# Performance work log

Measured on AMD Instinct MI355X. Metric: run time of the kernel, lower is better.

## Reference

```python
import jax, jax.numpy as jnp
import numpy as np

D_IN, D_HID, D_CLS, N_CLASSES = 1024, 256, 128, 4
CELL_IN = 512
N = 50000


def setup_inputs() -> dict:
    key = jax.random.key(0)
    ks = jax.random.split(key, 20)
    s = 0.02
    inp = {
        "x_path": jax.random.normal(ks[0], (1, N, D_IN), jnp.float32),
        "x_cell": jax.random.normal(ks[1], (1, N, CELL_IN), jnp.float32),
        # wsi_net / cell_net projections
        "wsi_w": jax.random.normal(ks[2], (D_IN, D_HID), jnp.float32) * s,
        "wsi_b": jnp.zeros((D_HID,), jnp.float32),
        "cell_w": jax.random.normal(ks[3], (CELL_IN, D_HID), jnp.float32) * s,
        "cell_b": jnp.zeros((D_HID,), jnp.float32),
        # cross-attention Q/K/V
        "wq_w": jax.random.normal(ks[4], (D_HID, D_HID), jnp.float32) * s,
        "wq_b": jnp.zeros((D_HID,), jnp.float32),
        "wk_w": jax.random.normal(ks[5], (D_HID, D_HID), jnp.float32) * s,
        "wk_b": jnp.zeros((D_HID,), jnp.float32),
        "wv_w": jax.random.normal(ks[6], (D_HID, D_HID), jnp.float32) * s,
        "wv_b": jnp.zeros((D_HID,), jnp.float32),
        # gated attention (L=D=256, n_classes=1)
        "aa_w": jax.random.normal(ks[7], (D_HID, D_HID), jnp.float32) * s,
        "aa_b": jnp.zeros((D_HID,), jnp.float32),
        "ab_w": jax.random.normal(ks[8], (D_HID, D_HID), jnp.float32) * s,
        "ab_b": jnp.zeros((D_HID,), jnp.float32),
        "ac_w": jax.random.normal(ks[9], (D_HID, 1), jnp.float32) * s,
        "ac_b": jnp.zeros((1,), jnp.float32),
        # classifier MLP
        "c1_w": jax.random.normal(ks[10], (D_HID, D_CLS), jnp.float32) * s,
        "c1_b": jnp.zeros((D_CLS,), jnp.float32),
        "c2_w": jax.random.normal(ks[11], (D_CLS, N_CLASSES), jnp.float32) * s,
        "c2_b": jnp.zeros((N_CLASSES,), jnp.float32),
    }
    return inp


def reference(x_path, x_cell, wsi_w, wsi_b, cell_w, cell_b,
              wq_w, wq_b, wk_w, wk_b, wv_w, wv_b,
              aa_w, aa_b, ab_w, ab_b, ac_w, ac_b,
              c1_w, c1_b, c2_w, c2_b):
    xp = x_path[0]            # (N, D_IN)
    xc = x_cell[0]            # (N, CELL_IN)
    # instance-level projections (dropout inactive at eval)
    h_path = jax.nn.relu(xp @ wsi_w + wsi_b)    # (N, d)
    h_cell = jax.nn.relu(xc @ cell_w + cell_b)  # (N, d)
    # cross attention with per-instance seq_len=1 (bmm over N singleton batches)
    q = h_cell @ wq_w + wq_b
    k = h_path @ wk_w + wk_b
    v = h_path @ wv_w + wv_b
    scores = (jnp.einsum('nd,nd->n', q, k) / jnp.sqrt(jnp.float32(q.shape[-1])))[:, None, None]  # (N,1,1)
    attn_w = jax.nn.softmax(scores, axis=-1)     # (N,1,1), trivially ones
    fused = attn_w[:, 0, :] * v                  # (N, d)
    # gated attention MIL pooling
    a = jnp.tanh(fused @ aa_w + aa_b)
    b = jax.nn.sigmoid(fused @ ab_w + ab_b)
    A = (a * b) @ ac_w + ac_b                    # (N, 1)
    A_t = A.T                                    # (1, N)
    pooled = jax.nn.softmax(A_t, axis=1) @ fused # (1, d)
    # classifier MLP
    risk = jax.nn.relu(pooled @ c1_w + c1_b) @ c2_w + c2_b  # (1, n_classes)
    return risk
```

## Files before the change

kernel.cpp:

```cpp
#include <hip/hip_runtime.h>
#include <hip/hip_bf16.h>
#include <math.h>

#define D_IN 1024
#define D_HID 256
#define D_CLS 128
#define N_CLASSES 4
#define N_INST 50000

#define NPAD 50176
#define G1I (NPAD / 32)
#define RG2 128
#define GB (NPAD / RG2)
#define PSTR 258
#define NEG_BIG (-1e30f)

#define ROWS 64
#define NBLK ((N_INST + ROWS - 1) / ROWS)
#define NB2 64
#define CHUNK ((NBLK + NB2 - 1) / NB2)

#define WS_W1T   0u
#define WS_WVT   524288u
#define WS_WAT   655360u
#define WS_WBT   786432u
#define WS_CNT   917504u
#define WS_P1    917760u
#define WS_H     1322304u
#define WS_NEED2 ((size_t)WS_H + 25690112u)
#define WS_P1F   917504u
#define WS_P2F   1724800u

typedef __attribute__((ext_vector_type(8))) short bf16x8;
typedef __attribute__((ext_vector_type(4))) float f32x4;

__device__ __forceinline__ short f2bf(float x) {
    __hip_bfloat16 h = __float2bfloat16(x);
    return *reinterpret_cast<short*>(&h);
}
__device__ __forceinline__ float fast_tanh(float x) {
    float e = __expf(2.f * x);
    return 1.f - 2.f * __builtin_amdgcn_rcpf(e + 1.f);
}
__device__ __forceinline__ float fast_sigmoid(float x) {
    return __builtin_amdgcn_rcpf(1.f + __expf(-x));
}
__device__ __forceinline__ bf16x8 cvt8(float4 a, float4 b) {
    bf16x8 r;
    r[0] = f2bf(a.x); r[1] = f2bf(a.y); r[2] = f2bf(a.z); r[3] = f2bf(a.w);
    r[4] = f2bf(b.x); r[5] = f2bf(b.y); r[6] = f2bf(b.z); r[7] = f2bf(b.w);
    return r;
}
__device__ __forceinline__ bf16x8 cvt8v(f32x4 a, f32x4 b) {
    bf16x8 r;
    r[0] = f2bf(a[0]); r[1] = f2bf(a[1]); r[2] = f2bf(a[2]); r[3] = f2bf(a[3]);
    r[4] = f2bf(b[0]); r[5] = f2bf(b[1]); r[6] = f2bf(b[2]); r[7] = f2bf(b[3]);
    return r;
}
__device__ __forceinline__ bf16x8 load_cvt8(const float* __restrict__ p) {
    return cvt8(*(const float4*)p, *(const float4*)(p + 4));
}
__device__ __forceinline__ void async_ld16(const float* g, float* l) {
    __builtin_amdgcn_global_load_lds(
        (const __attribute__((address_space(1))) void*)g,
        (__attribute__((address_space(3))) void*)l, 16, 0, 0);
}

__global__ void convert_weights(const float* __restrict__ w1, const float* __restrict__ wv,
                                const float* __restrict__ wa, const float* __restrict__ wb,
                                __hip_bfloat16* __restrict__ w1t, __hip_bfloat16* __restrict__ wvt,
                                __hip_bfloat16* __restrict__ wat, __hip_bfloat16* __restrict__ wbt,
                                int frag) {
    __shared__ __hip_bfloat16 T[64][68];
    int b = blockIdx.x, tid = threadIdx.x;
    if (frag && b < 64) {
        const int group = tid >> 6, lane = tid & 63;
        const int colb = lane & 15;
        const int kb = (lane >> 4) * 8;
#pragma unroll
        for (int p = 0; p < 2; p++) {
            int tile = b * 8 + group * 2 + p;
            int kc = tile >> 4, w = (tile >> 2) & 3, ct = tile & 3;
            int col = w * 64 + ct * 16 + colb;
            const float* s = w1 + (size_t)(kc * 32 + kb) * D_HID + col;
            bf16x8 o;
#pragma unroll
            for (int j = 0; j < 8; j++) o[j] = f2bf(s[(size_t)j * D_HID]);
            *(bf16x8*)(w1t + (size_t)tile * 512 + lane * 8) = o;
        }
        return;
    }
    const float* src; __hip_bfloat16* dst; int K, tr, tc;
    if (b < 64) { src = w1; dst = w1t; K = D_IN; tr = b >> 2; tc = b & 3; }
    else {
        int m = (b - 64) >> 4, t = (b - 64) & 15;
        src = (m == 0) ? wv : (m == 1) ? wa : wb;
        dst = (m == 0) ? wvt : (m == 1) ? wat : wbt;
        K = D_HID; tr = t >> 2; tc = t & 3;
    }
    int k0 = tr * 64, n0 = tc * 64;
#pragma unroll
    for (int p = 0; p < 4; p++) {
        int lin = p * 256 + tid;
        int r = lin >> 4;
        int c4 = (lin & 15) << 2;
        float4 v = *(const float4*)(src + (size_t)(k0 + r) * D_HID + n0 + c4);
        T[c4 + 0][r] = __float2bfloat16(v.x);
        T[c4 + 1][r] = __float2bfloat16(v.y);
        T[c4 + 2][r] = __float2bfloat16(v.z);
        T[c4 + 3][r] = __float2bfloat16(v.w);
    }
    __syncthreads();
#pragma unroll
    for (int p = 0; p < 4; p++) {
        int lin = p * 256 + tid;
        int n = lin >> 4;
        int kq = (lin & 15) << 2;
        ushort4 o;
        o.x = *(unsigned short*)&T[n][kq + 0];
        o.y = *(unsigned short*)&T[n][kq + 1];
        o.z = *(unsigned short*)&T[n][kq + 2];
        o.w = *(unsigned short*)&T[n][kq + 3];
        *(ushort4*)(dst + (size_t)(n0 + n) * K + k0 + kq) = o;
    }
}

__global__ __launch_bounds__(256, 5) void mcat_stage1i(const float* __restrict__ xp,
                                                       const __hip_bfloat16* __restrict__ w1f,
                                                       const float* __restrict__ b1,
                                                       __hip_bfloat16* __restrict__ hout) {
    __shared__ float Xs[4][1024];

    const int tid  = threadIdx.x;
    const int wave = tid >> 6;
    const int lane = tid & 63;
    const int quad = lane >> 4;
    const int l16  = lane & 15;
    const int row0 = blockIdx.x * 32;
    const int t128 = blockIdx.x >> 2;
    const int qtr  = blockIdx.x & 3;

    const int rsub = lane >> 3;
    const int gran = (lane & 7) ^ rsub;
    const float* xsrc;
    {
        int rg = row0 + wave * 8 + rsub;
        if (rg > N_INST - 1) rg = N_INST - 1;
        xsrc = xp + (size_t)rg * D_IN + gran * 4;
    }

    const __hip_bfloat16* wbase = w1f + (size_t)wave * 4 * 512 + lane * 8;

    f32x4 acc[2][4];
    f32x4 zero = {0.f, 0.f, 0.f, 0.f};
#pragma unroll
    for (int i = 0; i < 2; i++)
#pragma unroll
        for (int j = 0; j < 4; j++) acc[i][j] = zero;

    async_ld16(xsrc + 0, &Xs[0][wave * 256]);
    bf16x8 wcur[4];
#pragma unroll
    for (int ct = 0; ct < 4; ct++) wcur[ct] = *(const bf16x8*)(wbase + (size_t)ct * 512);
    async_ld16(xsrc + 32, &Xs[1][wave * 256]);
    async_ld16(xsrc + 64, &Xs[2][wave * 256]);

    const int key = l16 & 7;
#pragma unroll 1
    for (int t = 0; t < 32; t++) {
        if (t == 0)      asm volatile("s_waitcnt vmcnt(2)" ::: "memory");
        else if (t < 29) asm volatile("s_waitcnt vmcnt(1)" ::: "memory");
        else             asm volatile("s_waitcnt vmcnt(0)" ::: "memory");
        __builtin_amdgcn_s_barrier();

        bf16x8 wnx[4];
        if (t < 31) {
#pragma unroll
            for (int ct = 0; ct < 4; ct++)
                wnx[ct] = *(const bf16x8*)(wbase + (size_t)((t + 1) * 16 + ct) * 512);
        }
        if (t < 29) async_ld16(xsrc + (t + 3) * 32, &Xs[(t + 3) & 3][wave * 256]);

        const float* bufp = &Xs[t & 3][0];
#pragma unroll
        for (int rt = 0; rt < 2; rt++) {
            const float* rp = bufp + (rt * 16 + l16) * 32;
            f32x4 lo = *(const f32x4*)(rp + (((2 * quad) ^ key) << 2));
            f32x4 hi = *(const f32x4*)(rp + (((2 * quad + 1) ^ key) << 2));
            bf16x8 af = cvt8v(lo, hi);
#pragma unroll
            for (int ct = 0; ct < 4; ct++)
                acc[rt][ct] = __builtin_amdgcn_mfma_f32_16x16x32_bf16(af, wcur[ct], acc[rt][ct], 0, 0, 0);
        }
        if (t < 31) {
#pragma unroll
            for (int ct = 0; ct < 4; ct++) wcur[ct] = wnx[ct];
        }
    }

#pragma unroll
    for (int ct = 0; ct < 4; ct++) {
        const int col = wave * 64 + ct * 16 + l16;
        const float bias = b1[col];
        __hip_bfloat16* hb = hout + (((size_t)(t128 * 8 + (col >> 5)) * 4 + ((col >> 3) & 3)) << 10)
                                  + qtr * 256 + (col & 7);
#pragma unroll
        for (int rt = 0; rt < 2; rt++)
#pragma unroll
            for (int r = 0; r < 4; r++) {
                int row = rt * 16 + quad * 4 + r;
                hb[row * 8] = __float2bfloat16(fmaxf(acc[rt][ct][r] + bias, 0.f));
            }
    }
}

__global__ __launch_bounds__(512, 1) void mcat_stage2(const __hip_bfloat16* __restrict__ h,
                          const __hip_bfloat16* __restrict__ wvt, const float* __restrict__ bv,
                          const __hip_bfloat16* __restrict__ wat, const float* __restrict__ ba,
                          const __hip_bfloat16* __restrict__ wbt, const float* __restrict__ bb,
                          const float* __restrict__ acw, const float* __restrict__ acb,
                          float* __restrict__ p1, unsigned int* __restrict__ counter,
                          const float* __restrict__ c1w, const float* __restrict__ c1b,
                          const float* __restrict__ c2w, const float* __restrict__ c2b,
                          float* __restrict__ out) {
    __shared__ __hip_bfloat16 Vs[RG2][264];
    __shared__ float Apart[8][RG2];
    __shared__ float ExpW[RG2];
    __shared__ float smx[4];
    __shared__ float scb[GB];
    __shared__ float pooled[D_HID];
    __shared__ float r1v[D_CLS];

    const int tid  = threadIdx.x;
    const int wave = tid >> 6;
    const int lane = tid & 63;
    const int quad = lane >> 4;
    const int l16  = lane & 15;
    const int cb   = wave * 32;
    const int row0 = blockIdx.x * RG2;

    f32x4 acc[8][2];
    f32x4 zero = {0.f, 0.f, 0.f, 0.f};

    const __hip_bfloat16* hb = h + (size_t)blockIdx.x * 32768 + quad * 1024 + l16 * 8;
#pragma unroll
    for (int i = 0; i < 8; i++) { acc[i][0] = zero; acc[i][1] = zero; }
    {
        const __hip_bfloat16* w0 = wvt + (size_t)(cb + l16) * D_HID + quad * 8;
        const __hip_bfloat16* w1p = w0 + 16 * D_HID;
#pragma unroll
        for (int ks = 0; ks < 8; ks++) {
            bf16x8 b0 = *(const bf16x8*)(w0 + ks * 32);
            bf16x8 b1f = *(const bf16x8*)(w1p + ks * 32);
#pragma unroll
            for (int rt = 0; rt < 8; rt++) {
                bf16x8 af = *(const bf16x8*)(hb + ks * 4096 + rt * 128);
                acc[rt][0] = __builtin_amdgcn_mfma_f32_16x16x32_bf16(af, b0, acc[rt][0], 0, 0, 0);
                acc[rt][1] = __builtin_amdgcn_mfma_f32_16x16x32_bf16(af, b1f, acc[rt][1], 0, 0, 0);
            }
        }
    }
#pragma unroll
    for (int ct = 0; ct < 2; ct++) {
        int col = cb + ct * 16 + l16;
        float bias = bv[col];
#pragma unroll
        for (int rt = 0; rt < 8; rt++)
#pragma unroll
            for (int r = 0; r < 4; r++)
                Vs[rt * 16 + quad * 4 + r][col] = __float2bfloat16(acc[rt][ct][r] + bias);
    }
    __syncthreads();

    float a_reg[8][2][4];
#pragma unroll
    for (int i = 0; i < 8; i++) { acc[i][0] = zero; acc[i][1] = zero; }
    {
        const __hip_bfloat16* w0 = wat + (size_t)(cb + l16) * D_HID + quad * 8;
        const __hip_bfloat16* w1p = w0 + 16 * D_HID;
#pragma unroll
        for (int ks = 0; ks < 8; ks++) {
            bf16x8 b0 = *(const bf16x8*)(w0 + ks * 32);
            bf16x8 b1f = *(const bf16x8*)(w1p + ks * 32);
#pragma unroll
            for (int rt = 0; rt < 8; rt++) {
                bf16x8 af = *(const bf16x8*)&Vs[rt * 16 + l16][ks * 32 + quad * 8];
                acc[rt][0] = __builtin_amdgcn_mfma_f32_16x16x32_bf16(af, b0, acc[rt][0], 0, 0, 0);
                acc[rt][1] = __builtin_amdgcn_mfma_f32_16x16x32_bf16(af, b1f, acc[rt][1], 0, 0, 0);
            }
        }
    }
#pragma unroll
    for (int ct = 0; ct < 2; ct++) {
        float bias = ba[cb + ct * 16 + l16];
#pragma unroll
        for (int rt = 0; rt < 8; rt++)
#pragma unroll
            for (int r = 0; r < 4; r++)
                a_reg[rt][ct][r] = fast_tanh(acc[rt][ct][r] + bias);
    }

#pragma unroll
    for (int i = 0; i < 8; i++) { acc[i][0] = zero; acc[i][1] = zero; }
    {
        const __hip_bfloat16* w0 = wbt + (size_t)(cb + l16) * D_HID + quad * 8;
        const __hip_bfloat16* w1p = w0 + 16 * D_HID;
#pragma unroll
        for (int ks = 0; ks < 8; ks++) {
            bf16x8 b0 = *(const bf16x8*)(w0 + ks * 32);
            bf16x8 b1f = *(const bf16x8*)(w1p + ks * 32);
#pragma unroll
            for (int rt = 0; rt < 8; rt++) {
                bf16x8 af = *(const bf16x8*)&Vs[rt * 16 + l16][ks * 32 + quad * 8];
                acc[rt][0] = __builtin_amdgcn_mfma_f32_16x16x32_bf16(af, b0, acc[rt][0], 0, 0, 0);
                acc[rt][1] = __builtin_amdgcn_mfma_f32_16x16x32_bf16(af, b1f, acc[rt][1], 0, 0, 0);
            }
        }
    }
    {
        float acw0 = acw[cb + l16], acw1 = acw[cb + 16 + l16];
        float bb0 = bb[cb + l16],  bb1 = bb[cb + 16 + l16];
        float sp[8][4];
#pragma unroll
        for (int rt = 0; rt < 8; rt++)
#pragma unroll
            for (int r = 0; r < 4; r++) {
                float g0 = a_reg[rt][0][r] * fast_sigmoid(acc[rt][0][r] + bb0);
                float g1 = a_reg[rt][1][r] * fast_sigmoid(acc[rt][1][r] + bb1);
                sp[rt][r] = g0 * acw0 + g1 * acw1;
            }
#pragma unroll
        for (int off = 1; off < 16; off <<= 1)
#pragma unroll
            for (int rt = 0; rt < 8; rt++)
#pragma unroll
                for (int r = 0; r < 4; r++)
                    sp[rt][r] += __shfl_xor(sp[rt][r], off, 16);
        if (l16 == 0) {
#pragma unroll
            for (int rt = 0; rt < 8; rt++)
#pragma unroll
                for (int r = 0; r < 4; r++)
                    Apart[wave][rt * 16 + quad * 4 + r] = sp[rt][r];
        }
    }
    __syncthreads();

    if (tid < 64) {
        float A0 = acb[0], A1 = acb[0];
#pragma unroll
        for (int w = 0; w < 8; w++) { A0 += Apart[w][tid]; A1 += Apart[w][tid + 64]; }
        bool v0 = (row0 + tid) < N_INST;
        bool v1 = (row0 + 64 + tid) < N_INST;
        if (!v0) A0 = NEG_BIG;
        if (!v1) A1 = NEG_BIG;
        float m = fmaxf(A0, A1);
#pragma unroll
        for (int off = 32; off > 0; off >>= 1) m = fmaxf(m, __shfl_xor(m, off));
        float e0 = v0 ? __expf(A0 - m) : 0.f;
        float e1 = v1 ? __expf(A1 - m) : 0.f;
        ExpW[tid] = e0; ExpW[tid + 64] = e1;
        float ssum = e0 + e1;
#pragma unroll
        for (int off = 32; off > 0; off >>= 1) ssum += __shfl_xor(ssum, off);
        if (tid == 0) {
            p1[(size_t)blockIdx.x * PSTR + 0] = m;
            p1[(size_t)blockIdx.x * PSTR + 1] = ssum;
        }
    }
    __syncthreads();
    if (tid < 256) {
        float p = 0.f;
#pragma unroll 8
        for (int n = 0; n < RG2; n++)
            p += ExpW[n] * __bfloat162float(Vs[n][tid]);
        p1[(size_t)blockIdx.x * PSTR + 2 + tid] = p;
    }

    __syncthreads();
    if (tid == 0) {
        __threadfence();
        unsigned int old = __hip_atomic_fetch_add(counter, 1u, __ATOMIC_ACQ_REL, __HIP_MEMORY_SCOPE_AGENT);
        smx[3] = (old == GB - 1) ? 1.f : 0.f;
    }
    __syncthreads();
    if (smx[3] == 0.f) return;
    __threadfence();

    {
        float mloc = NEG_BIG;
        for (int b = tid; b < GB; b += 512) mloc = fmaxf(mloc, p1[(size_t)b * PSTR]);
#pragma unroll
        for (int off = 32; off > 0; off >>= 1) mloc = fmaxf(mloc, __shfl_xor(mloc, off));
        if (lane == 0) ExpW[wave] = mloc;
    }
    __syncthreads();
    if (tid == 0) {
        float M = NEG_BIG;
#pragma unroll
        for (int w = 0; w < 8; w++) M = fmaxf(M, ExpW[w]);
        smx[0] = M;
    }
    __syncthreads();
    {
        float M = smx[0];
        float sl = 0.f;
        for (int b = tid; b < GB; b += 512) {
            float s = __expf(p1[(size_t)b * PSTR] - M);
            scb[b] = s;
            sl += s * p1[(size_t)b * PSTR + 1];
        }
#pragma unroll
        for (int off = 32; off > 0; off >>= 1) sl += __shfl_xor(sl, off);
        if (lane == 0) ExpW[8 + wave] = sl;
    }
    __syncthreads();
    if (tid == 0) {
        float S = 0.f;
#pragma unroll
        for (int w = 0; w < 8; w++) S += ExpW[8 + w];
        smx[1] = S;
    }
    __syncthreads();
    if (tid < 256) {
        float p = 0.f;
        for (int b = 0; b < GB; b++)
            p += scb[b] * p1[(size_t)b * PSTR + 2 + tid];
        pooled[tid] = p / smx[1];
    }
    __syncthreads();
    if (tid < D_CLS) {
        float a2 = c1b[tid];
#pragma unroll 8
        for (int d = 0; d < D_HID; d++)
            a2 += pooled[d] * c1w[(size_t)d * D_CLS + tid];
        r1v[tid] = fmaxf(a2, 0.f);
    }
    __syncthreads();
    if (tid < N_CLASSES) {
        float a2 = c2b[tid];
#pragma unroll 8
        for (int j = 0; j < D_CLS; j++)
            a2 += r1v[j] * c2w[(size_t)j * N_CLASSES + tid];
        out[tid] = a2;
    }
}

__device__ __forceinline__ void gemm256_w8(const __hip_bfloat16 (*S)[264],
                                           const __hip_bfloat16* __restrict__ Wt,
                                           int colbase, int quad, int l16, f32x4 acc[4][2]) {
    f32x4 zero = {0.f, 0.f, 0.f, 0.f};
#pragma unroll
    for (int i = 0; i < 4; i++) { acc[i][0] = zero; acc[i][1] = zero; }
    const __hip_bfloat16* w0 = Wt + (size_t)(colbase + l16) * D_HID + quad * 8;
    const __hip_bfloat16* w1 = w0 + 16 * D_HID;
#pragma unroll
    for (int ks = 0; ks < 8; ks++) {
        bf16x8 af[4];
#pragma unroll
        for (int rt = 0; rt < 4; rt++)
            af[rt] = *(const bf16x8*)&S[rt * 16 + l16][ks * 32 + quad * 8];
        bf16x8 b0 = *(const bf16x8*)(w0 + ks * 32);
        bf16x8 b1 = *(const bf16x8*)(w1 + ks * 32);
#pragma unroll
        for (int rt = 0; rt < 4; rt++) {
            acc[rt][0] = __builtin_amdgcn_mfma_f32_16x16x32_bf16(af[rt], b0, acc[rt][0], 0, 0, 0);
            acc[rt][1] = __builtin_amdgcn_mfma_f32_16x16x32_bf16(af[rt], b1, acc[rt][1], 0, 0, 0);
        }
    }
}

__global__ __launch_bounds__(512, 4) void mcat_mainF(const float* __restrict__ xsrc,
                          const __hip_bfloat16* __restrict__ w1t, const float* __restrict__ b1,
                          const __hip_bfloat16* __restrict__ wvt, const float* __restrict__ bv,
                          const __hip_bfloat16* __restrict__ wat, const float* __restrict__ ba,
                          const __hip_bfloat16* __restrict__ wbt, const float* __restrict__ bb,
                          const float* __restrict__ acw, const float* __restrict__ acb,
                          float* __restrict__ partials) {
    __shared__ __hip_bfloat16 Hs[ROWS][264];
    __shared__ __hip_bfloat16 Vs[ROWS][264];
    __shared__ float Apart[8][ROWS];
    __shared__ float ExpW[ROWS];
    const int tid  = threadIdx.x;
    const int wave = tid >> 6;
    const int lane = tid & 63;
    const int quad = lane >> 4;
    const int l16  = lane & 15;
    const int colbase = wave * 32;
    const int row0 = blockIdx.x * ROWS;
    f32x4 acc[4][2];
    f32x4 zero = {0.f, 0.f, 0.f, 0.f};
#pragma unroll
    for (int i = 0; i < 4; i++) { acc[i][0] = zero; acc[i][1] = zero; }
    const float* xf_base[4];
#pragma unroll
    for (int rt = 0; rt < 4; rt++) {
        int r = row0 + rt * 16 + l16;
        if (r > N_INST - 1) r = N_INST - 1;
        xf_base[rt] = xsrc + (size_t)r * D_IN + quad * 8;
    }
    const __hip_bfloat16* wb0 = w1t + (size_t)(colbase + l16) * D_IN + quad * 8;
    const __hip_bfloat16* wb1 = wb0 + 16 * D_IN;
    for (int kc = 0; kc < D_IN; kc += 32) {
        bf16x8 af[4];
#pragma unroll
        for (int rt = 0; rt < 4; rt++) af[rt] = load_cvt8(xf_base[rt] + kc);
        bf16x8 b0 = *(const bf16x8*)(wb0 + kc);
        bf16x8 b1 = *(const bf16x8*)(wb1 + kc);
#pragma unroll
        for (int rt = 0; rt < 4; rt++) {
            acc[rt][0] = __builtin_amdgcn_mfma_f32_16x16x32_bf16(af[rt], b0, acc[rt][0], 0, 0, 0);
            acc[rt][1] = __builtin_amdgcn_mfma_f32_16x16x32_bf16(af[rt], b1, acc[rt][1], 0, 0, 0);
        }
    }
#pragma unroll
    for (int ct = 0; ct < 2; ct++) {
        int col = colbase + ct * 16 + l16;
        float bias = b1[col];
#pragma unroll
        for (int rt = 0; rt < 4; rt++)
#pragma unroll
            for (int r = 0; r < 4; r++)
                Hs[rt * 16 + quad * 4 + r][col] = __float2bfloat16(fmaxf(acc[rt][ct][r] + bias, 0.f));
    }
    __syncthreads();
    gemm256_w8(Hs, wvt, colbase, quad, l16, acc);
#pragma unroll
    for (int ct = 0; ct < 2; ct++) {
        int col = colbase + ct * 16 + l16;
        float bias = bv[col];
#pragma unroll
        for (int rt = 0; rt < 4; rt++)
#pragma unroll
            for (int r = 0; r < 4; r++)
                Vs[rt * 16 + quad * 4 + r][col] = __float2bfloat16(acc[rt][ct][r] + bias);
    }
    __syncthreads();
    float a_reg[4][2][4];
    gemm256_w8(Vs, wat, colbase, quad, l16, acc);
#pragma unroll
    for (int ct = 0; ct < 2; ct++) {
        float bias = ba[colbase + ct * 16 + l16];
#pragma unroll
        for (int rt = 0; rt < 4; rt++)
#pragma unroll
            for (int r = 0; r < 4; r++)
                a_reg[rt][ct][r] = fast_tanh(acc[rt][ct][r] + bias);
    }
    gemm256_w8(Vs, wbt, colbase, quad, l16, acc);
    {
        float acw0 = acw[colbase + l16];
        float acw1 = acw[colbase + 16 + l16];
        float bias0 = bb[colbase + l16];
        float bias1 = bb[colbase + 16 + l16];
        float sp[4][4];
#pragma unroll
        for (int rt = 0; rt < 4; rt++)
#pragma unroll
            for (int r = 0; r < 4; r++) {
                float g0 = a_reg[rt][0][r] * fast_sigmoid(acc[rt][0][r] + bias0);
                float g1 = a_reg[rt][1][r] * fast_sigmoid(acc[rt][1][r] + bias1);
                sp[rt][r] = g0 * acw0 + g1 * acw1;
            }
#pragma unroll
        for (int off = 1; off < 16; off <<= 1)
#pragma unroll
            for (int rt = 0; rt < 4; rt++)
#pragma unroll
                for (int r = 0; r < 4; r++)
                    sp[rt][r] += __shfl_xor(sp[rt][r], off, 16);
        if (l16 == 0) {
#pragma unroll
            for (int rt = 0; rt < 4; rt++)
#pragma unroll
                for (int r = 0; r < 4; r++)
                    Apart[wave][rt * 16 + quad * 4 + r] = sp[rt][r];
        }
    }
    __syncthreads();
    if (tid < 64) {
        bool valid = (row0 + tid) < N_INST;
        float A = acb[0];
#pragma unroll
        for (int w = 0; w < 8; w++) A += Apart[w][tid];
        if (!valid) A = NEG_BIG;
        float m = A;
#pragma unroll
        for (int off = 32; off > 0; off >>= 1) m = fmaxf(m, __shfl_xor(m, off));
        float e = valid ? __expf(A - m) : 0.f;
        ExpW[tid] = e;
        float ssum = e;
#pragma unroll
        for (int off = 32; off > 0; off >>= 1) ssum += __shfl_xor(ssum, off);
        if (tid == 0) {
            partials[(size_t)blockIdx.x * PSTR + 0] = m;
            partials[(size_t)blockIdx.x * PSTR + 1] = ssum;
        }
    }
    __syncthreads();
    if (tid < 256) {
        float p = 0.f;
#pragma unroll 8
        for (int n = 0; n < 64; n++)
            p += ExpW[n] * __bfloat162float(Vs[n][tid]);
        partials[(size_t)blockIdx.x * PSTR + 2 + tid] = p;
    }
}

__global__ void mcat_fin_a(const float* __restrict__ p1, float* __restrict__ p2) {
    __shared__ float sm[1];
    int g = blockIdx.x, tid = threadIdx.x;
    int lo = g * CHUNK;
    int hi = lo + CHUNK; if (hi > NBLK) hi = NBLK;
    if (tid < 64) {
        float m = NEG_BIG;
        if (lo + tid < hi) m = p1[(size_t)(lo + tid) * PSTR];
#pragma unroll
        for (int off = 32; off > 0; off >>= 1) m = fmaxf(m, __shfl_xor(m, off));
        if (tid == 0) sm[0] = m;
    }
    __syncthreads();
    float M = sm[0];
    float p = 0.f, sacc = 0.f;
    for (int b = lo; b < hi; b++) {
        float sc = __expf(p1[(size_t)b * PSTR] - M);
        sacc += sc * p1[(size_t)b * PSTR + 1];
        p += sc * p1[(size_t)b * PSTR + 2 + tid];
    }
    if (tid == 0) {
        p2[(size_t)g * PSTR + 0] = M;
        p2[(size_t)g * PSTR + 1] = sacc;
    }
    p2[(size_t)g * PSTR + 2 + tid] = p;
}

__global__ void mcat_fin_b(const float* __restrict__ p2,
                           const float* __restrict__ c1w, const float* __restrict__ c1b,
                           const float* __restrict__ c2w, const float* __restrict__ c2b,
                           float* __restrict__ out) {
    __shared__ float sm[2];
    __shared__ float sc[NB2];
    __shared__ float pooled[D_HID];
    __shared__ float r1[D_CLS];
    int tid = threadIdx.x;
    if (tid < 64) {
        float m = p2[(size_t)tid * PSTR];
#pragma unroll
        for (int off = 32; off > 0; off >>= 1) m = fmaxf(m, __shfl_xor(m, off));
        if (tid == 0) sm[0] = m;
    }
    __syncthreads();
    float M = sm[0];
    if (tid < 64) {
        float s = __expf(p2[(size_t)tid * PSTR] - M);
        sc[tid] = s;
        float Ssum = s * p2[(size_t)tid * PSTR + 1];
#pragma unroll
        for (int off = 32; off > 0; off >>= 1) Ssum += __shfl_xor(Ssum, off);
        if (tid == 0) sm[1] = Ssum;
    }
    __syncthreads();
    float S = sm[1];
    float p = 0.f;
#pragma unroll 8
    for (int b = 0; b < NB2; b++)
        p += sc[b] * p2[(size_t)b * PSTR + 2 + tid];
    pooled[tid] = p / S;
    __syncthreads();
    if (tid < D_CLS) {
        float acc = c1b[tid];
#pragma unroll 8
        for (int d = 0; d < D_HID; d++)
            acc += pooled[d] * c1w[(size_t)d * D_CLS + tid];
        r1[tid] = fmaxf(acc, 0.f);
    }
    __syncthreads();
    if (tid < N_CLASSES) {
        float acc = c2b[tid];
#pragma unroll 8
        for (int j = 0; j < D_CLS; j++)
            acc += r1[j] * c2w[(size_t)j * N_CLASSES + tid];
        out[tid] = acc;
    }
}

extern "C" void kernel_launch(void* const* d_in, const int* in_sizes, int n_in,
                              void* d_out, int out_size, void* d_ws, size_t ws_size,
                              hipStream_t stream) {
    const float* xp  = (const float*)d_in[0];
    const float* w1  = (const float*)d_in[2];
    const float* b1  = (const float*)d_in[3];
    const float* wv  = (const float*)d_in[10];
    const float* bv  = (const float*)d_in[11];
    const float* wa  = (const float*)d_in[12];
    const float* ba  = (const float*)d_in[13];
    const float* wb  = (const float*)d_in[14];
    const float* bb  = (const float*)d_in[15];
    const float* acw = (const float*)d_in[16];
    const float* acb = (const float*)d_in[17];
    const float* c1w = (const float*)d_in[18];
    const float* c1b = (const float*)d_in[19];
    const float* c2w = (const float*)d_in[20];
    const float* c2b = (const float*)d_in[21];
    float* out = (float*)d_out;

    char* ws = (char*)d_ws;
    __hip_bfloat16* w1t = (__hip_bfloat16*)(ws + WS_W1T);
    __hip_bfloat16* wvt = (__hip_bfloat16*)(ws + WS_WVT);
    __hip_bfloat16* wat = (__hip_bfloat16*)(ws + WS_WAT);
    __hip_bfloat16* wbt = (__hip_bfloat16*)(ws + WS_WBT);

    const int use_main = (ws_size >= WS_NEED2) ? 1 : 0;
    hipLaunchKernelGGL(convert_weights, dim3(112), dim3(256), 0, stream,
                       w1, wv, wa, wb, w1t, wvt, wat, wbt, use_main);

    if (use_main) {
        unsigned int* counter = (unsigned int*)(ws + WS_CNT);
        float* p1 = (float*)(ws + WS_P1);
        __hip_bfloat16* h  = (__hip_bfloat16*)(ws + WS_H);
        hipMemsetAsync(counter, 0, 4, stream);
        hipLaunchKernelGGL(mcat_stage1i, dim3(G1I), dim3(256), 0, stream, xp, w1t, b1, h);
        hipLaunchKernelGGL(mcat_stage2, dim3(GB), dim3(512), 0, stream,
                           h, wvt, bv, wat, ba, wbt, bb, acw, acb, p1, counter,
                           c1w, c1b, c2w, c2b, out);
    } else {
        float* p1 = (float*)(ws + WS_P1F);
        float* p2 = (float*)(ws + WS_P2F);
        hipLaunchKernelGGL(mcat_mainF, dim3(NBLK), dim3(512), 0, stream,
                           xp, w1t, b1, wvt, bv, wat, ba, wbt, bb, acw, acb, p1);
        hipLaunchKernelGGL(mcat_fin_a, dim3(NB2), dim3(256), 0, stream, p1, p2);
        hipLaunchKernelGGL(mcat_fin_b, dim3(1), dim3(256), 0, stream,
                           p2, c1w, c1b, c2w, c2b, out);
    }
}
```

Baseline: 509.7 us.

## Fuse stage1 projection with V/gate stages into one 32-row kernel

Merges the two-kernel main path into a single kernel. Each 32-row block now computes relu(x@W1), keeps H in shared memory, then runs the V, tanh and sigmoid gate projections and the per-block softmax partials. This removes the bf16 H round trip through global memory and one launch. In exchange it uses more LDS and registers (occupancy hint lowered to 3), repeats the small-weight loads in 4x more blocks, and makes the last-block final reduction handle 4x more partials.

After: 583.3 us. 14.4% more time.

```diff
diff --git a/kernel.cpp b/kernel.cpp
--- a/kernel.cpp
+++ b/kernel.cpp
@@ -10,8 +10,6 @@
 
 #define NPAD 50176
 #define G1I (NPAD / 32)
-#define RG2 128
-#define GB (NPAD / RG2)
 #define PSTR 258
 #define NEG_BIG (-1e30f)
 
@@ -26,8 +24,7 @@
 #define WS_WBT   786432u
 #define WS_CNT   917504u
 #define WS_P1    917760u
-#define WS_H     1322304u
-#define WS_NEED2 ((size_t)WS_H + 25690112u)
+#define WS_NEEDF ((size_t)WS_P1 + 1618176u)
 #define WS_P1F   917504u
 #define WS_P2F   1724800u
 
@@ -73,20 +70,28 @@
                                 int frag) {
     __shared__ __hip_bfloat16 T[64][68];
     int b = blockIdx.x, tid = threadIdx.x;
-    if (frag && b < 64) {
+    if (frag) {
         const int group = tid >> 6, lane = tid & 63;
         const int colb = lane & 15;
         const int kb = (lane >> 4) * 8;
+        const float* src; __hip_bfloat16* dst; int tbase;
+        if (b < 64) { src = w1; dst = w1t; tbase = b * 8; }
+        else {
+            int m = (b - 64) >> 4;
+            src = (m == 0) ? wv : (m == 1) ? wa : wb;
+            dst = (m == 0) ? wvt : (m == 1) ? wat : wbt;
+            tbase = ((b - 64) & 15) * 8;
+        }
 #pragma unroll
         for (int p = 0; p < 2; p++) {
-            int tile = b * 8 + group * 2 + p;
+            int tile = tbase + group * 2 + p;
             int kc = tile >> 4, w = (tile >> 2) & 3, ct = tile & 3;
             int col = w * 64 + ct * 16 + colb;
-            const float* s = w1 + (size_t)(kc * 32 + kb) * D_HID + col;
+            const float* s = src + (size_t)(kc * 32 + kb) * D_HID + col;
             bf16x8 o;
 #pragma unroll
             for (int j = 0; j < 8; j++) o[j] = f2bf(s[(size_t)j * D_HID]);
-            *(bf16x8*)(w1t + (size_t)tile * 512 + lane * 8) = o;
+            *(bf16x8*)(dst + (size_t)tile * 512 + lane * 8) = o;
         }
         return;
     }
@@ -125,11 +130,26 @@
     }
 }
 
-__global__ __launch_bounds__(256, 5) void mcat_stage1i(const float* __restrict__ xp,
-                                                       const __hip_bfloat16* __restrict__ w1f,
-                                                       const float* __restrict__ b1,
-                                                       __hip_bfloat16* __restrict__ hout) {
-    __shared__ float Xs[4][1024];
+__global__ __launch_bounds__(256, 3) void mcat_fused(const float* __restrict__ xp,
+                          const __hip_bfloat16* __restrict__ w1f, const float* __restrict__ b1,
+                          const __hip_bfloat16* __restrict__ wvf, const float* __restrict__ bv,
+                          const __hip_bfloat16* __restrict__ waf, const float* __restrict__ ba,
+                          const __hip_bfloat16* __restrict__ wbf, const float* __restrict__ bbp,
+                          const float* __restrict__ acw, const float* __restrict__ acb,
+                          float* __restrict__ p1, unsigned int* __restrict__ counter,
+                          const float* __restrict__ c1w, const float* __restrict__ c1b,
+                          const float* __restrict__ c2w, const float* __restrict__ c2b,
+                          float* __restrict__ out) {
+    __shared__ __align__(16) char smem[50832];
+    float (*Xs)[1024]          = (float (*)[1024])smem;
+    __hip_bfloat16 (*Hs)[264]  = (__hip_bfloat16 (*)[264])(smem + 16384);
+    __hip_bfloat16 (*Vsh)[264] = (__hip_bfloat16 (*)[264])(smem + 33280);
+    float (*Apart)[32]         = (float (*)[32])(smem + 50176);
+    float* ExpW = (float*)(smem + 50688);
+    float* smx  = (float*)(smem + 50816);
+    float* scb    = (float*)smem;
+    float* pooled = (float*)(smem + 8192);
+    float* r1v    = (float*)(smem + 9216);
 
     const int tid  = threadIdx.x;
     const int wave = tid >> 6;
@@ -137,8 +157,7 @@
     const int quad = lane >> 4;
     const int l16  = lane & 15;
     const int row0 = blockIdx.x * 32;
-    const int t128 = blockIdx.x >> 2;
-    const int qtr  = blockIdx.x & 3;
+    const int colb = wave * 64;
 
     const int rsub = lane >> 3;
     const int gran = (lane & 7) ^ rsub;
@@ -148,7 +167,6 @@
         if (rg > N_INST - 1) rg = N_INST - 1;
         xsrc = xp + (size_t)rg * D_IN + gran * 4;
     }
-
     const __hip_bfloat16* wbase = w1f + (size_t)wave * 4 * 512 + lane * 8;
 
     f32x4 acc[2][4];
@@ -200,145 +218,131 @@
 
 #pragma unroll
     for (int ct = 0; ct < 4; ct++) {
-        const int col = wave * 64 + ct * 16 + l16;
+        const int col = colb + ct * 16 + l16;
         const float bias = b1[col];
-        __hip_bfloat16* hb = hout + (((size_t)(t128 * 8 + (col >> 5)) * 4 + ((col >> 3) & 3)) << 10)
-                                  + qtr * 256 + (col & 7);
 #pragma unroll
         for (int rt = 0; rt < 2; rt++)
 #pragma unroll
+            for (int r = 0; r < 4; r++)
+                Hs[rt * 16 + quad * 4 + r][col] = __float2bfloat16(fmaxf(acc[rt][ct][r] + bias, 0.f));
+    }
+    __syncthreads();
+
+    f32x4 vacc[2][4];
+#pragma unroll
+    for (int i = 0; i < 2; i++)
+#pragma unroll
+        for (int j = 0; j < 4; j++) vacc[i][j] = zero;
+    {
+        const __hip_bfloat16* wvb = wvf + (size_t)wave * 4 * 512 + lane * 8;
+#pragma unroll
+        for (int kc = 0; kc < 8; kc++) {
+            bf16x8 wfr[4];
+#pragma unroll
+            for (int ct = 0; ct < 4; ct++)
+                wfr[ct] = *(const bf16x8*)(wvb + (size_t)(kc * 16 + ct) * 512);
+#pragma unroll
+            for (int rt = 0; rt < 2; rt++) {
+                bf16x8 af = *(const bf16x8*)&Hs[rt * 16 + l16][kc * 32 + quad * 8];
+#pragma unroll
+                for (int ct = 0; ct < 4; ct++)
+                    vacc[rt][ct] = __builtin_amdgcn_mfma_f32_16x16x32_bf16(af, wfr[ct], vacc[rt][ct], 0, 0, 0);
+            }
+        }
+    }
+#pragma unroll
+    for (int ct = 0; ct < 4; ct++) {
+        const int col = colb + ct * 16 + l16;
+        const float bias = bv[col];
+#pragma unroll
+        for (int rt = 0; rt < 2; rt++)
+#pragma unroll
+            for (int r = 0; r < 4; r++)
+                Vsh[rt * 16 + quad * 4 + r][col] = __float2bfloat16(vacc[rt][ct][r] + bias);
+    }
+    __syncthreads();
+
+#pragma unroll
+    for (int i = 0; i < 2; i++)
+#pragma unroll
+        for (int j = 0; j < 4; j++) vacc[i][j] = zero;
+    {
+        const __hip_bfloat16* wab = waf + (size_t)wave * 4 * 512 + lane * 8;
+#pragma unroll
+        for (int kc = 0; kc < 8; kc++) {
+            bf16x8 wfr[4];
+#pragma unroll
+            for (int ct = 0; ct < 4; ct++)
+                wfr[ct] = *(const bf16x8*)(wab + (size_t)(kc * 16 + ct) * 512);
+#pragma unroll
+            for (int rt = 0; rt < 2; rt++) {
+                bf16x8 af = *(const bf16x8*)&Vsh[rt * 16 + l16][kc * 32 + quad * 8];
+#pragma unroll
+                for (int ct = 0; ct < 4; ct++)
+                    vacc[rt][ct] = __builtin_amdgcn_mfma_f32_16x16x32_bf16(af, wfr[ct], vacc[rt][ct], 0, 0, 0);
+            }
+        }
+    }
+    float a_reg[2][4][4];
+#pragma unroll
+    for (int ct = 0; ct < 4; ct++) {
+        const float bias = ba[colb + ct * 16 + l16];
+#pragma unroll
+        for (int rt = 0; rt < 2; rt++)
+#pragma unroll
+            for (int r = 0; r < 4; r++)
+                a_reg[rt][ct][r] = fast_tanh(vacc[rt][ct][r] + bias);
+    }
+
+#pragma unroll
+    for (int i = 0; i < 2; i++)
+#pragma unroll
+        for (int j = 0; j < 4; j++) vacc[i][j] = zero;
+    {
+        const __hip_bfloat16* wbb = wbf + (size_t)wave * 4 * 512 + lane * 8;
+#pragma unroll
+        for (int kc = 0; kc < 8; kc++) {
+            bf16x8 wfr[4];
+#pragma unroll
+            for (int ct = 0; ct < 4; ct++)
+                wfr[ct] = *(const bf16x8*)(wbb + (size_t)(kc * 16 + ct) * 512);
+#pragma unroll
+            for (int rt = 0; rt < 2; rt++) {
+                bf16x8 af = *(const bf16x8*)&Vsh[rt * 16 + l16][kc * 32 + quad * 8];
+#pragma unroll
+                for (int ct = 0; ct < 4; ct++)
+                    vacc[rt][ct] = __builtin_amdgcn_mfma_f32_16x16x32_bf16(af, wfr[ct], vacc[rt][ct], 0, 0, 0);
+            }
+        }
+    }
+    {
+        float acwv[4], bbv[4];
+#pragma unroll
+        for (int ct = 0; ct < 4; ct++) {
+            acwv[ct] = acw[colb + ct * 16 + l16];
+            bbv[ct]  = bbp[colb + ct * 16 + l16];
+        }
+        float sp[2][4];
+#pragma unroll
+        for (int rt = 0; rt < 2; rt++)
+#pragma unroll
             for (int r = 0; r < 4; r++) {
-                int row = rt * 16 + quad * 4 + r;
-                hb[row * 8] = __float2bfloat16(fmaxf(acc[rt][ct][r] + bias, 0.f));
+                float s = 0.f;
+#pragma unroll
+                for (int ct = 0; ct < 4; ct++)
+                    s += a_reg[rt][ct][r] * fast_sigmoid(vacc[rt][ct][r] + bbv[ct]) * acwv[ct];
+                sp[rt][r] = s;
             }
-    }
-}
-
-__global__ __launch_bounds__(512, 1) void mcat_stage2(const __hip_bfloat16* __restrict__ h,
-                          const __hip_bfloat16* __restrict__ wvt, const float* __restrict__ bv,
-                          const __hip_bfloat16* __restrict__ wat, const float* __restrict__ ba,
-                          const __hip_bfloat16* __restrict__ wbt, const float* __restrict__ bb,
-                          const float* __restrict__ acw, const float* __restrict__ acb,
-                          float* __restrict__ p1, unsigned int* __restrict__ counter,
-                          const float* __restrict__ c1w, const float* __restrict__ c1b,
-                          const float* __restrict__ c2w, const float* __restrict__ c2b,
-                          float* __restrict__ out) {
-    __shared__ __hip_bfloat16 Vs[RG2][264];
-    __shared__ float Apart[8][RG2];
-    __shared__ float ExpW[RG2];
-    __shared__ float smx[4];
-    __shared__ float scb[GB];
-    __shared__ float pooled[D_HID];
-    __shared__ float r1v[D_CLS];
-
-    const int tid  = threadIdx.x;
-    const int wave = tid >> 6;
-    const int lane = tid & 63;
-    const int quad = lane >> 4;
-    const int l16  = lane & 15;
-    const int cb   = wave * 32;
-    const int row0 = blockIdx.x * RG2;
-
-    f32x4 acc[8][2];
-    f32x4 zero = {0.f, 0.f, 0.f, 0.f};
-
-    const __hip_bfloat16* hb = h + (size_t)blockIdx.x * 32768 + quad * 1024 + l16 * 8;
-#pragma unroll
-    for (int i = 0; i < 8; i++) { acc[i][0] = zero; acc[i][1] = zero; }
-    {
-        const __hip_bfloat16* w0 = wvt + (size_t)(cb + l16) * D_HID + quad * 8;
-        const __hip_bfloat16* w1p = w0 + 16 * D_HID;
-#pragma unroll
-        for (int ks = 0; ks < 8; ks++) {
-            bf16x8 b0 = *(const bf16x8*)(w0 + ks * 32);
-            bf16x8 b1f = *(const bf16x8*)(w1p + ks * 32);
-#pragma unroll
-            for (int rt = 0; rt < 8; rt++) {
-                bf16x8 af = *(const bf16x8*)(hb + ks * 4096 + rt * 128);
-                acc[rt][0] = __builtin_amdgcn_mfma_f32_16x16x32_bf16(af, b0, acc[rt][0], 0, 0, 0);
-                acc[rt][1] = __builtin_amdgcn_mfma_f32_16x16x32_bf16(af, b1f, acc[rt][1], 0, 0, 0);
-            }
-        }
-    }
-#pragma unroll
-    for (int ct = 0; ct < 2; ct++) {
-        int col = cb + ct * 16 + l16;
-        float bias = bv[col];
-#pragma unroll
-        for (int rt = 0; rt < 8; rt++)
-#pragma unroll
-            for (int r = 0; r < 4; r++)
-                Vs[rt * 16 + quad * 4 + r][col] = __float2bfloat16(acc[rt][ct][r] + bias);
-    }
-    __syncthreads();
-
-    float a_reg[8][2][4];
-#pragma unroll
-    for (int i = 0; i < 8; i++) { acc[i][0] = zero; acc[i][1] = zero; }
-    {
-        const __hip_bfloat16* w0 = wat + (size_t)(cb + l16) * D_HID + quad * 8;
-        const __hip_bfloat16* w1p = w0 + 16 * D_HID;
-#pragma unroll
-        for (int ks = 0; ks < 8; ks++) {
-            bf16x8 b0 = *(const bf16x8*)(w0 + ks * 32);
-            bf16x8 b1f = *(const bf16x8*)(w1p + ks * 32);
-#pragma unroll
-            for (int rt = 0; rt < 8; rt++) {
-                bf16x8 af = *(const bf16x8*)&Vs[rt * 16 + l16][ks * 32 + quad * 8];
-                acc[rt][0] = __builtin_amdgcn_mfma_f32_16x16x32_bf16(af, b0, acc[rt][0], 0, 0, 0);
-                acc[rt][1] = __builtin_amdgcn_mfma_f32_16x16x32_bf16(af, b1f, acc[rt][1], 0, 0, 0);
-            }
-        }
-    }
-#pragma unroll
-    for (int ct = 0; ct < 2; ct++) {
-        float bias = ba[cb + ct * 16 + l16];
-#pragma unroll
-        for (int rt = 0; rt < 8; rt++)
-#pragma unroll
-            for (int r = 0; r < 4; r++)
-                a_reg[rt][ct][r] = fast_tanh(acc[rt][ct][r] + bias);
-    }
-
-#pragma unroll
-    for (int i = 0; i < 8; i++) { acc[i][0] = zero; acc[i][1] = zero; }
-    {
-        const __hip_bfloat16* w0 = wbt + (size_t)(cb + l16) * D_HID + quad * 8;
-        const __hip_bfloat16* w1p = w0 + 16 * D_HID;
-#pragma unroll
-        for (int ks = 0; ks < 8; ks++) {
-            bf16x8 b0 = *(const bf16x8*)(w0 + ks * 32);
-            bf16x8 b1f = *(const bf16x8*)(w1p + ks * 32);
-#pragma unroll
-            for (int rt = 0; rt < 8; rt++) {
-                bf16x8 af = *(const bf16x8*)&Vs[rt * 16 + l16][ks * 32 + quad * 8];
-                acc[rt][0] = __builtin_amdgcn_mfma_f32_16x16x32_bf16(af, b0, acc[rt][0], 0, 0, 0);
-                acc[rt][1] = __builtin_amdgcn_mfma_f32_16x16x32_bf16(af, b1f, acc[rt][1], 0, 0, 0);
-            }
-        }
-    }
-    {
-        float acw0 = acw[cb + l16], acw1 = acw[cb + 16 + l16];
-        float bb0 = bb[cb + l16],  bb1 = bb[cb + 16 + l16];
-        float sp[8][4];
-#pragma unroll
-        for (int rt = 0; rt < 8; rt++)
-#pragma unroll
-            for (int r = 0; r < 4; r++) {
-                float g0 = a_reg[rt][0][r] * fast_sigmoid(acc[rt][0][r] + bb0);
-                float g1 = a_reg[rt][1][r] * fast_sigmoid(acc[rt][1][r] + bb1);
-                sp[rt][r] = g0 * acw0 + g1 * acw1;
-            }
 #pragma unroll
         for (int off = 1; off < 16; off <<= 1)
 #pragma unroll
-            for (int rt = 0; rt < 8; rt++)
+            for (int rt = 0; rt < 2; rt++)
 #pragma unroll
                 for (int r = 0; r < 4; r++)
                     sp[rt][r] += __shfl_xor(sp[rt][r], off, 16);
         if (l16 == 0) {
 #pragma unroll
-            for (int rt = 0; rt < 8; rt++)
+            for (int rt = 0; rt < 2; rt++)
 #pragma unroll
                 for (int r = 0; r < 4; r++)
                     Apart[wave][rt * 16 + quad * 4 + r] = sp[rt][r];
@@ -346,34 +350,31 @@
     }
     __syncthreads();
 
-    if (tid < 64) {
-        float A0 = acb[0], A1 = acb[0];
-#pragma unroll
-        for (int w = 0; w < 8; w++) { A0 += Apart[w][tid]; A1 += Apart[w][tid + 64]; }
-        bool v0 = (row0 + tid) < N_INST;
-        bool v1 = (row0 + 64 + tid) < N_INST;
-        if (!v0) A0 = NEG_BIG;
-        if (!v1) A1 = NEG_BIG;
-        float m = fmaxf(A0, A1);
-#pragma unroll
-        for (int off = 32; off > 0; off >>= 1) m = fmaxf(m, __shfl_xor(m, off));
-        float e0 = v0 ? __expf(A0 - m) : 0.f;
-        float e1 = v1 ? __expf(A1 - m) : 0.f;
-        ExpW[tid] = e0; ExpW[tid + 64] = e1;
-        float ssum = e0 + e1;
-#pragma unroll
-        for (int off = 32; off > 0; off >>= 1) ssum += __shfl_xor(ssum, off);
+    if (tid < 32) {
+        float A = acb[0];
+#pragma unroll
+        for (int w = 0; w < 4; w++) A += Apart[w][tid];
+        bool valid = (row0 + tid) < N_INST;
+        if (!valid) A = NEG_BIG;
+        float m = A;
+#pragma unroll
+        for (int off = 16; off > 0; off >>= 1) m = fmaxf(m, __shfl_xor(m, off, 32));
+        float e = valid ? __expf(A - m) : 0.f;
+        ExpW[tid] = e;
+        float ssum = e;
+#pragma unroll
+        for (int off = 16; off > 0; off >>= 1) ssum += __shfl_xor(ssum, off, 32);
         if (tid == 0) {
             p1[(size_t)blockIdx.x * PSTR + 0] = m;
             p1[(size_t)blockIdx.x * PSTR + 1] = ssum;
         }
     }
     __syncthreads();
-    if (tid < 256) {
+    {
         float p = 0.f;
 #pragma unroll 8
-        for (int n = 0; n < RG2; n++)
-            p += ExpW[n] * __bfloat162float(Vs[n][tid]);
+        for (int n = 0; n < 32; n++)
+            p += ExpW[n] * __bfloat162float(Vsh[n][tid]);
         p1[(size_t)blockIdx.x * PSTR + 2 + tid] = p;
     }
 
@@ -381,7 +382,7 @@
     if (tid == 0) {
         __threadfence();
         unsigned int old = __hip_atomic_fetch_add(counter, 1u, __ATOMIC_ACQ_REL, __HIP_MEMORY_SCOPE_AGENT);
-        smx[3] = (old == GB - 1) ? 1.f : 0.f;
+        smx[3] = (old == G1I - 1) ? 1.f : 0.f;
     }
     __syncthreads();
     if (smx[3] == 0.f) return;
@@ -389,7 +390,7 @@
 
     {
         float mloc = NEG_BIG;
-        for (int b = tid; b < GB; b += 512) mloc = fmaxf(mloc, p1[(size_t)b * PSTR]);
+        for (int b = tid; b < G1I; b += 256) mloc = fmaxf(mloc, p1[(size_t)b * PSTR]);
 #pragma unroll
         for (int off = 32; off > 0; off >>= 1) mloc = fmaxf(mloc, __shfl_xor(mloc, off));
         if (lane == 0) ExpW[wave] = mloc;
@@ -398,14 +399,14 @@
     if (tid == 0) {
         float M = NEG_BIG;
 #pragma unroll
-        for (int w = 0; w < 8; w++) M = fmaxf(M, ExpW[w]);
+        for (int w = 0; w < 4; w++) M = fmaxf(M, ExpW[w]);
         smx[0] = M;
     }
     __syncthreads();
     {
         float M = smx[0];
         float sl = 0.f;
-        for (int b = tid; b < GB; b += 512) {
+        for (int b = tid; b < G1I; b += 256) {
             float s = __expf(p1[(size_t)b * PSTR] - M);
             scb[b] = s;
             sl += s * p1[(size_t)b * PSTR + 1];
@@ -418,13 +419,13 @@
     if (tid == 0) {
         float S = 0.f;
 #pragma unroll
-        for (int w = 0; w < 8; w++) S += ExpW[8 + w];
+        for (int w = 0; w < 4; w++) S += ExpW[8 + w];
         smx[1] = S;
     }
     __syncthreads();
-    if (tid < 256) {
+    {
         float p = 0.f;
-        for (int b = 0; b < GB; b++)
+        for (int b = 0; b < G1I; b++)
             p += scb[b] * p1[(size_t)b * PSTR + 2 + tid];
         pooled[tid] = p / smx[1];
     }
@@ -710,18 +711,16 @@
     __hip_bfloat16* wat = (__hip_bfloat16*)(ws + WS_WAT);
     __hip_bfloat16* wbt = (__hip_bfloat16*)(ws + WS_WBT);
 
-    const int use_main = (ws_size >= WS_NEED2) ? 1 : 0;
+    const int use_main = (ws_size >= WS_NEEDF) ? 1 : 0;
     hipLaunchKernelGGL(convert_weights, dim3(112), dim3(256), 0, stream,
                        w1, wv, wa, wb, w1t, wvt, wat, wbt, use_main);
 
     if (use_main) {
         unsigned int* counter = (unsigned int*)(ws + WS_CNT);
         float* p1 = (float*)(ws + WS_P1);
-        __hip_bfloat16* h  = (__hip_bfloat16*)(ws + WS_H);
         hipMemsetAsync(counter, 0, 4, stream);
-        hipLaunchKernelGGL(mcat_stage1i, dim3(G1I), dim3(256), 0, stream, xp, w1t, b1, h);
-        hipLaunchKernelGGL(mcat_stage2, dim3(GB), dim3(512), 0, stream,
-                           h, wvt, bv, wat, ba, wbt, bb, acw, acb, p1, counter,
+        hipLaunchKernelGGL(mcat_fused, dim3(G1I), dim3(256), 0, stream,
+                           xp, w1t, b1, wvt, bv, wat, ba, wbt, bb, acw, acb, p1, counter,
                            c1w, c1b, c2w, c2b, out);
     } else {
         float* p1 = (float*)(ws + WS_P1F);
```
